# Optimization experiments

Hardware: AMD Instinct MI355X
Metric: run time of the kernel (lower is better)

## Reference

```python
import jax, jax.numpy as jnp
import numpy as np

G = 3040      # number of drugs / graph nodes in the drug-drug graph
A = 100       # atoms per molecular graph (smileNode, uniform)
TOK = 43      # token vocabulary (hard-coded in module)
FS = 75       # nfeat_smile
HS = 128      # nhid_smile
H1S = 128     # nhid1_smile
NF = 512      # nfeat (raw 384 + 128 smile emb)
NH = 256      # nhid
DH = 256      # dhid1


def setup_inputs() -> dict:
    key = jax.random.key(0)
    ks = jax.random.split(key, 20)
    s = 0.05
    inp = {
        "x": jax.random.normal(ks[0], (G, NF - H1S), dtype=jnp.float32),
        "adj_pos": jax.random.uniform(ks[1], (G, G), dtype=jnp.float32) / G,
        "adj_neg": jax.random.uniform(ks[2], (G, G), dtype=jnp.float32) / G,
        "mol_adj": jax.random.uniform(ks[3], (G, A, A), dtype=jnp.float32) / A,
        "encoded_drug": jax.random.randint(ks[4], (G, A), 0, TOK, dtype=jnp.int64),
        # learned params
        "tok_emb": jax.random.normal(ks[5], (TOK, FS), dtype=jnp.float32),
        "Wm1": jax.random.normal(ks[6], (G, FS, HS), dtype=jnp.float32) * s,
        "Wm2": jax.random.normal(ks[7], (G, HS, H1S), dtype=jnp.float32) * s,
        "Wp1": jax.random.normal(ks[8], (NF, NH), dtype=jnp.float32) * s,
        "Wp2": jax.random.normal(ks[9], (NH, NH), dtype=jnp.float32) * s,
        "Wn1": jax.random.normal(ks[10], (NF, NH), dtype=jnp.float32) * s,
        "Wn2": jax.random.normal(ks[11], (NH, NH), dtype=jnp.float32) * s,
        "Wd1": jax.random.normal(ks[12], (2 * NH, DH), dtype=jnp.float32) * s,
        "Wd2": jax.random.normal(ks[13], (DH, 2 * DH), dtype=jnp.float32) * s,
        "Wd3": jax.random.normal(ks[14], (2 * DH, DH), dtype=jnp.float32) * s,
        "Wdec": jax.random.normal(ks[15], (DH, DH), dtype=jnp.float32) * s,
    }
    return inp


def reference(x, adj_pos, adj_neg, mol_adj, encoded_drug, tok_emb,
              Wm1, Wm2, Wp1, Wp2, Wn1, Wn2, Wd1, Wd2, Wd3, Wdec):
    # --- calDrugSmileFeatures: batched over all 3040 per-graph GCN encoders ---
    feats = tok_emb[encoded_drug]                          # [G, A, FS] (embedding gather)
    h = jnp.einsum('gab,gaf,gfh->gbh', mol_adj, feats, Wm1)  # gc1: adj @ (x @ W1), per graph
    h = jnp.einsum('gab,gah,ghk->gbk', mol_adj, h, Wm2)      # gc2 (dropout inactive, eval)
    emb_drugs = jnp.max(h, axis=1)                          # [G, H1S] node-wise maxpool

    # --- main drug-drug graph ---
    xc = jnp.concatenate([x, emb_drugs], axis=1)            # [G, NF]
    hp = jax.nn.relu(adj_pos @ (xc @ Wp1))                  # GCNEncoder pos layer1
    zp = adj_pos @ (hp @ Wp2)                               # layer2
    hn = jax.nn.relu(adj_neg @ (xc @ Wn1))
    zn = adj_neg @ (hn @ Wn2)
    z = jnp.concatenate([zp, zn], axis=1)                   # [G, 2*NH]

    # --- DSN MLP (eval: dropout inactive) ---
    z = jax.nn.relu(z @ Wd1)
    z = jax.nn.relu(z @ Wd2)
    z = z @ Wd3                                             # [G, DH]

    # --- Bilinear decoder: z W z^T logits ---
    y_pred = (z @ Wdec) @ z.T                               # [G, G]
    return y_pred
```

## Files before the change

kernel.cpp:

```cpp
#include <hip/hip_runtime.h>
#include <cstdint>
#include <cstddef>

#define Gn   3040
#define An   100
#define TOKn 43
#define FSn  75
#define NFn  512
#define XC   384

typedef __attribute__((ext_vector_type(8))) short s16x8;
typedef __attribute__((ext_vector_type(4))) float f32x4;

__device__ __forceinline__ void split_bf16(float x, unsigned short &h, unsigned short &l)
{
  unsigned u = __float_as_uint(x);
  unsigned r = (u + 0x7fffu + ((u >> 16) & 1u)) & 0xffff0000u;
  h = (unsigned short)(r >> 16);
  float res = x - __uint_as_float(r);
  unsigned v = __float_as_uint(res);
  l = (unsigned short)((v + 0x7fffu + ((v >> 16) & 1u)) >> 16);
}

#define MFMA3(acc, ah, al, bh, bl)                                              \
  acc = __builtin_amdgcn_mfma_f32_16x16x32_bf16(ah, bh, acc, 0, 0, 0);          \
  acc = __builtin_amdgcn_mfma_f32_16x16x32_bf16(ah, bl, acc, 0, 0, 0);          \
  acc = __builtin_amdgcn_mfma_f32_16x16x32_bf16(al, bh, acc, 0, 0, 0);

__device__ __forceinline__ s16x8 tail_frag(const unsigned short* p, bool act)
{
  s16x8 f = {0,0,0,0,0,0,0,0};
  if (act) {
    uint2 v = *(const uint2*)p;
    f[0] = (short)(v.x & 0xffffu); f[1] = (short)(v.x >> 16);
    f[2] = (short)(v.y & 0xffffu); f[3] = (short)(v.y >> 16);
  }
  return f;
}

__device__ __forceinline__ void pack_split4(const f32x4 a, uint2 &ph, uint2 &pl)
{
  unsigned short h[4], l[4];
  #pragma unroll
  for (int r = 0; r < 4; ++r) split_bf16(a[r], h[r], l[r]);
  ph.x = (unsigned)h[0] | ((unsigned)h[1] << 16);
  ph.y = (unsigned)h[2] | ((unsigned)h[3] << 16);
  pl.x = (unsigned)l[0] | ((unsigned)l[1] << 16);
  pl.y = (unsigned)l[2] | ((unsigned)l[3] << 16);
}

__global__ void prep_tok_kernel(const float* __restrict__ tok_emb,
                                unsigned short* __restrict__ th,
                                unsigned short* __restrict__ tl)
{
  int i = blockIdx.x * 256 + threadIdx.x;
  if (i >= TOKn * 96) return;
  int r = i / 96, f = i % 96;
  float v = (f < FSn) ? tok_emb[r * FSn + f] : 0.f;
  unsigned short h, l;
  split_bf16(v, h, l);
  th[i] = h; tl[i] = l;
}

__global__ __launch_bounds__(256) void prep_w_kernel(
    const float* __restrict__ Wp1, const float* __restrict__ Wn1,
    const float* __restrict__ Wp2, const float* __restrict__ Wn2,
    const float* __restrict__ Wd1, const float* __restrict__ Wd2,
    const float* __restrict__ Wd3, const float* __restrict__ Wdec,
    unsigned short* __restrict__ WS)
{
  __shared__ float sT[32][33];
  const float* S; int K, N; unsigned off;
  switch (blockIdx.z) {
    case 0:  S = Wp1;  K = 512; N = 256; off = 0;       break;
    case 1:  S = Wn1;  K = 512; N = 256; off = 262144;  break;
    case 2:  S = Wp2;  K = 256; N = 256; off = 524288;  break;
    case 3:  S = Wn2;  K = 256; N = 256; off = 655360;  break;
    case 4:  S = Wd1;  K = 512; N = 256; off = 786432;  break;
    case 5:  S = Wd2;  K = 256; N = 512; off = 1048576; break;
    case 6:  S = Wd3;  K = 512; N = 256; off = 1310720; break;
    default: S = Wdec; K = 256; N = 256; off = 1572864; break;
  }
  const int r0 = blockIdx.x * 32, c0 = blockIdx.y * 32;
  if (r0 >= K || c0 >= N) return;
  unsigned short* H = WS + off;
  unsigned short* L = H + K * N;
  const int t = threadIdx.x;
  {
    const int i = t >> 3, j0 = (t & 7) * 4;
    float4 v = *(const float4*)&S[(size_t)(r0 + i) * N + c0 + j0];
    sT[i][j0] = v.x; sT[i][j0+1] = v.y; sT[i][j0+2] = v.z; sT[i][j0+3] = v.w;
  }
  __syncthreads();
  {
    const int jj = t >> 3, ii0 = (t & 7) * 4;
    unsigned short h[4], lo[4];
    #pragma unroll
    for (int q = 0; q < 4; ++q) split_bf16(sT[ii0 + q][jj], h[q], lo[q]);
    ushort4 hv = make_ushort4(h[0], h[1], h[2], h[3]);
    ushort4 lv = make_ushort4(lo[0], lo[1], lo[2], lo[3]);
    *(ushort4*)&H[(size_t)(c0 + jj) * K + r0 + ii0] = hv;
    *(ushort4*)&L[(size_t)(c0 + jj) * K + r0 + ii0] = lv;
  }
}

__global__ __launch_bounds__(1024, 1) void smile_mfma_kernel(
    const float* __restrict__ mol_adj, const int* __restrict__ enc,
    const unsigned short* __restrict__ tokh, const unsigned short* __restrict__ tokl,
    const float* __restrict__ Wm1, const float* __restrict__ Wm2,
    float* __restrict__ xc)
{
  __shared__ __align__(16) unsigned short sm[74624];
  __shared__ float sMax[8][2][16];
  unsigned short* adjT_h = sm;
  unsigned short* adjT_l = sm + 10400;
  unsigned short* bufA_h = sm + 20800;
  unsigned short* bufA_l = sm + 34112;
  unsigned short* g1_h   = sm + 47424;
  unsigned short* g1_l   = sm + 61024;
  float* Sf = (float*)(sm + 20800);

  const int g = blockIdx.x;
  const int t = threadIdx.x;
  const int w = t >> 6, l = t & 63;
  const int wc = w & 7, wr = w >> 3;
  const int lr = l & 15, lq = l >> 4;
  const int hcol = 16 * wc + lr;
  const int NI = wr ? 3 : 4;
  const int IB = wr * 4;
  const f32x4 z4 = {0.f, 0.f, 0.f, 0.f};
  const s16x8 z8 = {0,0,0,0,0,0,0,0};

  const float* adjg = mol_adj + (size_t)g * (An * An);
  #pragma unroll
  for (int j = 0; j < 3; ++j) {
    const int i = t + 1024 * j;
    if (i < 2500) {
      float4 v = *(const float4*)&adjg[i * 4];
      const int a = i / 25, c4 = (i % 25) * 4;
      float* p = &Sf[a * 101 + c4];
      p[0] = v.x; p[1] = v.y; p[2] = v.z; p[3] = v.w;
    }
  }
  __syncthreads();
  #pragma unroll
  for (int j = 0; j < 3; ++j) {
    const int i = t + 1024 * j;
    if (i < 2500) {
      const int b = i / 25, a4 = (i % 25) * 4;
      f32x4 v;
      #pragma unroll
      for (int q = 0; q < 4; ++q) v[q] = Sf[(a4 + q) * 101 + b];
      uint2 ph, pl;
      pack_split4(v, ph, pl);
      *(uint2*)&adjT_h[b * 104 + a4] = ph;
      *(uint2*)&adjT_l[b * 104 + a4] = pl;
    }
  }
  __syncthreads();

  {
    const float* W1 = Wm1 + (size_t)g * (FSn * 128);
    s16x8 bh[3], bl[3];
    #pragma unroll
    for (int kc = 0; kc < 3; ++kc)
      #pragma unroll
      for (int j = 0; j < 8; ++j) {
        const int f = 32 * kc + 8 * lq + j;
        float v = (f < FSn) ? W1[f * 128 + hcol] : 0.f;
        unsigned short hh, ll;
        split_bf16(v, hh, ll);
        bh[kc][j] = (short)hh; bl[kc][j] = (short)ll;
      }
    f32x4 acc[4];
    #pragma unroll
    for (int i = 0; i < 4; ++i) acc[i] = z4;
    #pragma unroll
    for (int m2 = 0; m2 < 4; ++m2) {
      if (m2 < NI) {
        const int mi = IB + m2;
        const int a = 16 * mi + lr;
        const bool va = a < An;
        const int tk = va ? enc[g * An + a] : 0;
        const unsigned short* th = tokh + tk * 96 + 8 * lq;
        const unsigned short* tl = tokl + tk * 96 + 8 * lq;
        #pragma unroll
        for (int kc = 0; kc < 3; ++kc) {
          s16x8 ah = z8, al = z8;
          if (va) { ah = *(const s16x8*)&th[32 * kc]; al = *(const s16x8*)&tl[32 * kc]; }
          MFMA3(acc[m2], ah, al, bh[kc], bl[kc]);
        }
      }
    }
    #pragma unroll
    for (int m2 = 0; m2 < 4; ++m2) {
      if (m2 < NI) {
        const int a0 = 16 * (IB + m2) + 4 * lq;
        if (a0 < An) {
          uint2 ph, pl;
          pack_split4(acc[m2], ph, pl);
          *(uint2*)&bufA_h[hcol * 104 + a0] = ph;
          *(uint2*)&bufA_l[hcol * 104 + a0] = pl;
        }
      }
    }
  }
  __syncthreads();

  {
    const unsigned short* xh = &bufA_h[hcol * 104];
    const unsigned short* xl = &bufA_l[hcol * 104];
    f32x4 acc[4];
    #pragma unroll
    for (int i = 0; i < 4; ++i) acc[i] = z4;
    #pragma unroll
    for (int kc = 0; kc < 4; ++kc) {
      s16x8 ah, al;
      if (kc < 3) {
        ah = *(const s16x8*)&xh[32 * kc + 8 * lq];
        al = *(const s16x8*)&xl[32 * kc + 8 * lq];
      } else {
        ah = tail_frag(xh + 96, lq == 0);
        al = tail_frag(xl + 96, lq == 0);
      }
      #pragma unroll
      for (int n2 = 0; n2 < 4; ++n2) {
        if (n2 < NI) {
          const int b = 16 * (IB + n2) + lr;
          const bool vb = b < An;
          s16x8 bh = z8, bl = z8;
          if (kc < 3) {
            if (vb) {
              bh = *(const s16x8*)&adjT_h[b * 104 + 32 * kc + 8 * lq];
              bl = *(const s16x8*)&adjT_l[b * 104 + 32 * kc + 8 * lq];
            }
          } else {
            bh = tail_frag(&adjT_h[b * 104 + 96], vb && lq == 0);
            bl = tail_frag(&adjT_l[b * 104 + 96], vb && lq == 0);
          }
          MFMA3(acc[n2], ah, al, bh, bl);
        }
      }
    }
    #pragma unroll
    for (int n2 = 0; n2 < 4; ++n2) {
      if (n2 < NI) {
        const int b = 16 * (IB + n2) + lr;
        if (b < An) {
          uint2 ph, pl;
          pack_split4(acc[n2], ph, pl);
          *(uint2*)&g1_h[b * 136 + 16 * wc + 4 * lq] = ph;
          *(uint2*)&g1_l[b * 136 + 16 * wc + 4 * lq] = pl;
        }
      }
    }
  }
  __syncthreads();

  {
    const float* W2 = Wm2 + (size_t)g * (128 * 128);
    s16x8 bh[4], bl[4];
    #pragma unroll
    for (int kc = 0; kc < 4; ++kc)
      #pragma unroll
      for (int j = 0; j < 8; ++j) {
        unsigned short hh, ll;
        split_bf16(W2[(32 * kc + 8 * lq + j) * 128 + hcol], hh, ll);
        bh[kc][j] = (short)hh; bl[kc][j] = (short)ll;
      }
    f32x4 acc[4];
    #pragma unroll
    for (int i = 0; i < 4; ++i) acc[i] = z4;
    #pragma unroll
    for (int kc = 0; kc < 4; ++kc) {
      #pragma unroll
      for (int m2 = 0; m2 < 4; ++m2) {
        if (m2 < NI) {
          const int b = 16 * (IB + m2) + lr;
          const bool vb = b < An;
          s16x8 ah = z8, al = z8;
          if (vb) {
            ah = *(const s16x8*)&g1_h[b * 136 + 32 * kc + 8 * lq];
            al = *(const s16x8*)&g1_l[b * 136 + 32 * kc + 8 * lq];
          }
          MFMA3(acc[m2], ah, al, bh[kc], bl[kc]);
        }
      }
    }
    #pragma unroll
    for (int m2 = 0; m2 < 4; ++m2) {
      if (m2 < NI) {
        const int b0 = 16 * (IB + m2) + 4 * lq;
        if (b0 < An) {
          uint2 ph, pl;
          pack_split4(acc[m2], ph, pl);
          *(uint2*)&bufA_h[hcol * 104 + b0] = ph;
          *(uint2*)&bufA_l[hcol * 104 + b0] = pl;
        }
      }
    }
  }
  __syncthreads();

  {
    const unsigned short* fh = &bufA_h[hcol * 104];
    const unsigned short* fl = &bufA_l[hcol * 104];
    f32x4 acc[4];
    #pragma unroll
    for (int i = 0; i < 4; ++i) acc[i] = z4;
    #pragma unroll
    for (int kc = 0; kc < 4; ++kc) {
      s16x8 ah, al;
      if (kc < 3) {
        ah = *(const s16x8*)&fh[32 * kc + 8 * lq];
        al = *(const s16x8*)&fl[32 * kc + 8 * lq];
      } else {
        ah = tail_frag(fh + 96, lq == 0);
        al = tail_frag(fl + 96, lq == 0);
      }
      #pragma unroll
      for (int n2 = 0; n2 < 4; ++n2) {
        if (n2 < NI) {
          const int b = 16 * (IB + n2) + lr;
          const bool vb = b < An;
          s16x8 bh = z8, bl = z8;
          if (kc < 3) {
            if (vb) {
              bh = *(const s16x8*)&adjT_h[b * 104 + 32 * kc + 8 * lq];
              bl = *(const s16x8*)&adjT_l[b * 104 + 32 * kc + 8 * lq];
            }
          } else {
            bh = tail_frag(&adjT_h[b * 104 + 96], vb && lq == 0);
            bl = tail_frag(&adjT_l[b * 104 + 96], vb && lq == 0);
          }
          MFMA3(acc[n2], ah, al, bh, bl);
        }
      }
    }
    float mr[4] = {-3.4e38f, -3.4e38f, -3.4e38f, -3.4e38f};
    #pragma unroll
    for (int n2 = 0; n2 < 4; ++n2) {
      if (n2 < NI && (16 * (IB + n2) + lr) < An) {
        #pragma unroll
        for (int r = 0; r < 4; ++r) mr[r] = fmaxf(mr[r], acc[n2][r]);
      }
    }
    #pragma unroll
    for (int d = 1; d < 16; d <<= 1) {
      #pragma unroll
      for (int r = 0; r < 4; ++r) mr[r] = fmaxf(mr[r], __shfl_xor(mr[r], d, 64));
    }
    if (lr == 0) {
      #pragma unroll
      for (int r = 0; r < 4; ++r) sMax[wc][wr][4 * lq + r] = mr[r];
    }
  }
  __syncthreads();
  if (wr == 0 && lr == 0) {
    #pragma unroll
    for (int r = 0; r < 4; ++r) {
      const int h = 16 * wc + 4 * lq + r;
      xc[(size_t)g * NFn + XC + h] =
          fmaxf(sMax[wc][0][4 * lq + r], sMax[wc][1][4 * lq + r]);
    }
  }
}

template<bool SPLIT, bool BF32>
__global__ __launch_bounds__(256, 2) void mgemm_kernel(
    const float* __restrict__ A0, const float* __restrict__ A1,
    const unsigned short* __restrict__ Bh0, const unsigned short* __restrict__ Bl0,
    const unsigned short* __restrict__ Bh1, const unsigned short* __restrict__ Bl1,
    const float* __restrict__ Bf,
    float* __restrict__ C0, float* __restrict__ C1,
    int M, int N, int K)
{
  __shared__ __align__(16) unsigned short lds[16384];

  const int z = blockIdx.z;
  int pair, k0base, kend;
  if (SPLIT) {
    pair = z & 1;
    int s = z >> 1;
    k0base = s * 768;
    kend = k0base + 768; if (kend > K) kend = K;
  } else { pair = 0; k0base = 0; kend = K; }

  const float* A = pair ? A1 : A0;
  const unsigned short* Bh = pair ? Bh1 : Bh0;
  const unsigned short* Bl = pair ? Bl1 : Bl0;
  float* C;
  if (SPLIT) C = (pair ? C1 : C0) + (size_t)(z >> 1) * M * N;
  else       C = C0;

  const int t  = threadIdx.x;
  const int l  = t & 63;
  const int wv = t >> 6;
  const int wr = wv >> 1, wc = wv & 1;
  const int m0 = blockIdx.x * 128, n0 = blockIdx.y * 128;

  const int sm = (t >> 6) * 16 + (t & 15);
  const int sk = ((t >> 4) & 3) * 8;

  const f32x4 zero4 = {0.f, 0.f, 0.f, 0.f};
  f32x4 acc[4][4];
  #pragma unroll
  for (int i = 0; i < 4; ++i)
    #pragma unroll
    for (int j = 0; j < 4; ++j) acc[i][j] = zero4;

  for (int k0 = k0base; k0 < kend; k0 += 32) {
    float4 a00 = make_float4(0.f,0.f,0.f,0.f), a01 = a00, a10 = a00, a11 = a00;
    {
      const size_t base = (size_t)(m0 + sm) * K + k0 + sk;
      if (m0 + sm < M)      { a00 = *(const float4*)&A[base];
                              a01 = *(const float4*)&A[base + 4]; }
      if (m0 + sm + 64 < M) { a10 = *(const float4*)&A[base + (size_t)64 * K];
                              a11 = *(const float4*)&A[base + (size_t)64 * K + 4]; }
    }
    s16x8 b0h, b0l, b1h, b1l;
    float4 bf00, bf01, bf10, bf11;
    if (BF32) {
      bf00 = make_float4(0.f,0.f,0.f,0.f); bf01 = bf00; bf10 = bf00; bf11 = bf00;
      const size_t base = (size_t)(n0 + sm) * K + k0 + sk;
      if (n0 + sm < N)      { bf00 = *(const float4*)&Bf[base];
                              bf01 = *(const float4*)&Bf[base + 4]; }
      if (n0 + sm + 64 < N) { bf10 = *(const float4*)&Bf[base + (size_t)64 * K];
                              bf11 = *(const float4*)&Bf[base + (size_t)64 * K + 4]; }
    } else {
      const size_t base = (size_t)(n0 + sm) * K + k0 + sk;
      b0h = *(const s16x8*)&Bh[base];
      b0l = *(const s16x8*)&Bl[base];
      b1h = *(const s16x8*)&Bh[base + (size_t)64 * K];
      b1l = *(const s16x8*)&Bl[base + (size_t)64 * K];
    }

    s16x8 a0h, a0l, a1h, a1l;
    {
      const float av0[8] = {a00.x,a00.y,a00.z,a00.w,a01.x,a01.y,a01.z,a01.w};
      const float av1[8] = {a10.x,a10.y,a10.z,a10.w,a11.x,a11.y,a11.z,a11.w};
      #pragma unroll
      for (int j = 0; j < 8; ++j) {
        unsigned short hh, ll;
        split_bf16(av0[j], hh, ll); a0h[j] = (short)hh; a0l[j] = (short)ll;
        split_bf16(av1[j], hh, ll); a1h[j] = (short)hh; a1l[j] = (short)ll;
      }
    }
    if (BF32) {
      const float bv0[8] = {bf00.x,bf00.y,bf00.z,bf00.w,bf01.x,bf01.y,bf01.z,bf01.w};
      const float bv1[8] = {bf10.x,bf10.y,bf10.z,bf10.w,bf11.x,bf11.y,bf11.z,bf11.w};
      #pragma unroll
      for (int j = 0; j < 8; ++j) {
        unsigned short hh, ll;
        split_bf16(bv0[j], hh, ll); b0h[j] = (short)hh; b0l[j] = (short)ll;
        split_bf16(bv1[j], hh, ll); b1h[j] = (short)hh; b1l[j] = (short)ll;
      }
    }

    __syncthreads();
    {
      const int sl = (t & 63) * 8;
      const int c1 = t >> 6, c2 = c1 + 4;
      *(s16x8*)&lds[c1 * 512 + sl]          = a0h;
      *(s16x8*)&lds[4096 + c1 * 512 + sl]   = a0l;
      *(s16x8*)&lds[c2 * 512 + sl]          = a1h;
      *(s16x8*)&lds[4096 + c2 * 512 + sl]   = a1l;
      *(s16x8*)&lds[8192  + c1 * 512 + sl]  = b0h;
      *(s16x8*)&lds[12288 + c1 * 512 + sl]  = b0l;
      *(s16x8*)&lds[8192  + c2 * 512 + sl]  = b1h;
      *(s16x8*)&lds[12288 + c2 * 512 + sl]  = b1l;
    }
    __syncthreads();

    s16x8 vbh[4], vbl[4];
    #pragma unroll
    for (int ni = 0; ni < 4; ++ni) {
      const int c = wc * 4 + ni;
      vbh[ni] = *(const s16x8*)&lds[8192  + c * 512 + l * 8];
      vbl[ni] = *(const s16x8*)&lds[12288 + c * 512 + l * 8];
    }
    #pragma unroll
    for (int mi = 0; mi < 4; ++mi) {
      const int c = wr * 4 + mi;
      s16x8 ah = *(const s16x8*)&lds[c * 512 + l * 8];
      s16x8 al = *(const s16x8*)&lds[4096 + c * 512 + l * 8];
      #pragma unroll
      for (int ni = 0; ni < 4; ++ni) {
        acc[mi][ni] = __builtin_amdgcn_mfma_f32_16x16x32_bf16(ah, vbh[ni], acc[mi][ni], 0, 0, 0);
        acc[mi][ni] = __builtin_amdgcn_mfma_f32_16x16x32_bf16(ah, vbl[ni], acc[mi][ni], 0, 0, 0);
        acc[mi][ni] = __builtin_amdgcn_mfma_f32_16x16x32_bf16(al, vbh[ni], acc[mi][ni], 0, 0, 0);
      }
    }
  }

  #pragma unroll
  for (int mi = 0; mi < 4; ++mi) {
    const int rowb = m0 + (wr * 4 + mi) * 16 + (l >> 4) * 4;
    #pragma unroll
    for (int ni = 0; ni < 4; ++ni) {
      const int col = n0 + (wc * 4 + ni) * 16 + (l & 15);
      if (col < N) {
        #pragma unroll
        for (int r = 0; r < 4; ++r) {
          const int row = rowb + r;
          if (row < M) C[(size_t)row * N + col] = acc[mi][ni][r];
        }
      }
    }
  }
}

template<int EOUT>
__global__ __launch_bounds__(256, 2) void wgemm_kernel(
    const float* __restrict__ A0, const float* __restrict__ A1,
    const unsigned short* __restrict__ Bh0, const unsigned short* __restrict__ Bl0,
    const unsigned short* __restrict__ Bh1, const unsigned short* __restrict__ Bl1,
    float* __restrict__ C0, float* __restrict__ C1,
    unsigned short* __restrict__ H0, unsigned short* __restrict__ L0,
    unsigned short* __restrict__ H1, unsigned short* __restrict__ L1,
    int M, int N, int K)
{
  __shared__ __align__(16) unsigned short lds[16384];

  const int pair = blockIdx.z;
  const float* A = pair ? A1 : A0;
  const unsigned short* Bh = pair ? Bh1 : Bh0;
  const unsigned short* Bl = pair ? Bl1 : Bl0;

  const int t  = threadIdx.x;
  const int l  = t & 63;
  const int wv = t >> 6;
  const int wr = wv >> 1, wc = wv & 1;
  const int m0 = blockIdx.x * 128, n0 = blockIdx.y * 128;

  const int sm = (t >> 6) * 16 + (t & 15);
  const int sk = ((t >> 4) & 3) * 8;

  const f32x4 zero4 = {0.f, 0.f, 0.f, 0.f};
  f32x4 acc[4][4];
  #pragma unroll
  for (int i = 0; i < 4; ++i)
    #pragma unroll
    for (int j = 0; j < 4; ++j) acc[i][j] = zero4;

  for (int k0 = 0; k0 < K; k0 += 32) {
    float4 a00 = make_float4(0.f,0.f,0.f,0.f), a01 = a00, a10 = a00, a11 = a00;
    {
      const size_t base = (size_t)(m0 + sm) * K + k0 + sk;
      if (m0 + sm < M)      { a00 = *(const float4*)&A[base];
                              a01 = *(const float4*)&A[base + 4]; }
      if (m0 + sm + 64 < M) { a10 = *(const float4*)&A[base + (size_t)64 * K];
                              a11 = *(const float4*)&A[base + (size_t)64 * K + 4]; }
    }
    s16x8 b0h, b0l, b1h, b1l;
    {
      const size_t base = (size_t)(n0 + sm) * K + k0 + sk;
      b0h = *(const s16x8*)&Bh[base];
      b0l = *(const s16x8*)&Bl[base];
      b1h = *(const s16x8*)&Bh[base + (size_t)64 * K];
      b1l = *(const s16x8*)&Bl[base + (size_t)64 * K];
    }
    s16x8 a0h, a0l, a1h, a1l;
    {
      const float av0[8] = {a00.x,a00.y,a00.z,a00.w,a01.x,a01.y,a01.z,a01.w};
      const float av1[8] = {a10.x,a10.y,a10.z,a10.w,a11.x,a11.y,a11.z,a11.w};
      #pragma unroll
      for (int j = 0; j < 8; ++j) {
        unsigned short hh, ll;
        split_bf16(av0[j], hh, ll); a0h[j] = (short)hh; a0l[j] = (short)ll;
        split_bf16(av1[j], hh, ll); a1h[j] = (short)hh; a1l[j] = (short)ll;
      }
    }

    __syncthreads();
    {
      const int sl = (t & 63) * 8;
      const int c1 = t >> 6, c2 = c1 + 4;
      *(s16x8*)&lds[c1 * 512 + sl]          = a0h;
      *(s16x8*)&lds[4096 + c1 * 512 + sl]   = a0l;
      *(s16x8*)&lds[c2 * 512 + sl]          = a1h;
      *(s16x8*)&lds[4096 + c2 * 512 + sl]   = a1l;
      *(s16x8*)&lds[8192  + c1 * 512 + sl]  = b0h;
      *(s16x8*)&lds[12288 + c1 * 512 + sl]  = b0l;
      *(s16x8*)&lds[8192  + c2 * 512 + sl]  = b1h;
      *(s16x8*)&lds[12288 + c2 * 512 + sl]  = b1l;
    }
    __syncthreads();

    s16x8 vbh[4], vbl[4];
    #pragma unroll
    for (int ni = 0; ni < 4; ++ni) {
      const int c = wc * 4 + ni;
      vbh[ni] = *(const s16x8*)&lds[8192  + c * 512 + l * 8];
      vbl[ni] = *(const s16x8*)&lds[12288 + c * 512 + l * 8];
    }
    #pragma unroll
    for (int mi = 0; mi < 4; ++mi) {
      const int c = wr * 4 + mi;
      s16x8 ah = *(const s16x8*)&lds[c * 512 + l * 8];
      s16x8 al = *(const s16x8*)&lds[4096 + c * 512 + l * 8];
      #pragma unroll
      for (int ni = 0; ni < 4; ++ni) {
        acc[mi][ni] = __builtin_amdgcn_mfma_f32_16x16x32_bf16(ah, vbh[ni], acc[mi][ni], 0, 0, 0);
        acc[mi][ni] = __builtin_amdgcn_mfma_f32_16x16x32_bf16(ah, vbl[ni], acc[mi][ni], 0, 0, 0);
        acc[mi][ni] = __builtin_amdgcn_mfma_f32_16x16x32_bf16(al, vbh[ni], acc[mi][ni], 0, 0, 0);
      }
    }
  }

  if (EOUT <= 1) {
    float* C = pair ? C1 : C0;
    #pragma unroll
    for (int mi = 0; mi < 4; ++mi) {
      const int rowb = m0 + (wr * 4 + mi) * 16 + (l >> 4) * 4;
      #pragma unroll
      for (int ni = 0; ni < 4; ++ni) {
        const int col = n0 + (wc * 4 + ni) * 16 + (l & 15);
        if (col < N) {
          #pragma unroll
          for (int r = 0; r < 4; ++r) {
            const int row = rowb + r;
            if (row < M) {
              float v = acc[mi][ni][r];
              if (EOUT == 1) v = fmaxf(v, 0.f);
              C[(size_t)row * N + col] = v;
            }
          }
        }
      }
    }
  } else {
    unsigned short* H = pair ? H1 : H0;
    unsigned short* L = pair ? L1 : L0;
    #pragma unroll
    for (int mi = 0; mi < 4; ++mi) {
      const int rowb = m0 + (wr * 4 + mi) * 16 + (l >> 4) * 4;
      if (rowb < M) {
        #pragma unroll
        for (int ni = 0; ni < 4; ++ni) {
          const int col = n0 + (wc * 4 + ni) * 16 + (l & 15);
          if (col < N) {
            uint2 ph, pl;
            pack_split4(acc[mi][ni], ph, pl);
            *(uint2*)&H[(size_t)col * M + rowb] = ph;
            *(uint2*)&L[(size_t)col * M + rowb] = pl;
          }
        }
      }
    }
  }
}

__global__ void reduce_kernel(const float* __restrict__ part, float* __restrict__ dst,
                              int S, int M, int N, int ldc, int coff, int relu)
{
  int i = blockIdx.x * blockDim.x + threadIdx.x;
  int total = M * (N / 4);
  if (i >= total) return;
  int r = i / (N / 4), c = (i % (N / 4)) * 4;
  float4 s = make_float4(0.f, 0.f, 0.f, 0.f);
  for (int j = 0; j < S; ++j) {
    float4 v = *(const float4*)&part[(size_t)j * M * N + (size_t)r * N + c];
    s.x += v.x; s.y += v.y; s.z += v.z; s.w += v.w;
  }
  if (relu) {
    s.x = fmaxf(s.x, 0.f); s.y = fmaxf(s.y, 0.f);
    s.z = fmaxf(s.z, 0.f); s.w = fmaxf(s.w, 0.f);
  }
  *(float4*)&dst[(size_t)r * ldc + coff + c] = s;
}

__global__ void copyx_kernel(const float* __restrict__ x, float* __restrict__ xc)
{
  int i = blockIdx.x * blockDim.x + threadIdx.x;
  int total = Gn * (XC / 4);
  if (i >= total) return;
  int r = i / (XC / 4), c = (i % (XC / 4)) * 4;
  *(float4*)&xc[(size_t)r * NFn + c] = *(const float4*)&x[(size_t)r * XC + c];
}

extern "C" void kernel_launch(void* const* d_in, const int* in_sizes, int n_in,
                              void* d_out, int out_size, void* d_ws, size_t ws_size,
                              hipStream_t stream)
{
  const float* x       = (const float*)d_in[0];
  const float* adj_pos = (const float*)d_in[1];
  const float* adj_neg = (const float*)d_in[2];
  const float* mol_adj = (const float*)d_in[3];
  const int*   enc     = (const int*)d_in[4];
  const float* tok_emb = (const float*)d_in[5];
  const float* Wm1     = (const float*)d_in[6];
  const float* Wm2     = (const float*)d_in[7];
  const float* Wp1     = (const float*)d_in[8];
  const float* Wp2     = (const float*)d_in[9];
  const float* Wn1     = (const float*)d_in[10];
  const float* Wn2     = (const float*)d_in[11];
  const float* Wd1     = (const float*)d_in[12];
  const float* Wd2     = (const float*)d_in[13];
  const float* Wd3     = (const float*)d_in[14];
  const float* Wdec    = (const float*)d_in[15];
  float* out = (float*)d_out;
  float* ws  = (float*)d_ws;

  const size_t MN  = (size_t)Gn * 256;
  const size_t MN2 = (size_t)Gn * 512;
  size_t o = 0;
  float* xc    = ws + o; o += MN2;
  float* P1    = ws + o; o += MN;
  float* N1    = ws + o; o += MN;
  float* hp    = ws + o; o += MN;
  float* hn    = ws + o; o += MN;
  float* P2    = ws + o; o += MN;
  float* N2    = ws + o; o += MN;
  float* zbuf  = ws + o; o += MN2;
  float* d1    = ws + o; o += MN;
  float* d2    = ws + o; o += MN2;
  float* z3    = ws + o; o += MN;
  float* tb    = ws + o; o += MN;
  float* partP = ws + o; o += 4 * MN;
  float* partN = ws + o; o += 4 * MN;
  unsigned short* tokh = (unsigned short*)(ws + o);
  unsigned short* tokl = tokh + TOKn * 96; o += 4128;
  unsigned short* WS = (unsigned short*)(ws + o); o += 851968;
  unsigned short* Wp1s  = WS + 0;
  unsigned short* Wn1s  = WS + 262144;
  unsigned short* Wp2s  = WS + 524288;
  unsigned short* Wn2s  = WS + 655360;
  unsigned short* Wd1s  = WS + 786432;
  unsigned short* Wd2s  = WS + 1048576;
  unsigned short* Wd3s  = WS + 1310720;
  unsigned short* Wdecs = WS + 1572864;

  unsigned short* BTPh = (unsigned short*)d2;
  unsigned short* BTPl = BTPh + (size_t)256 * Gn;
  unsigned short* BTNh = BTPh + (size_t)2 * 256 * Gn;
  unsigned short* BTNl = BTPh + (size_t)3 * 256 * Gn;

  dim3 b256(256);

  prep_tok_kernel<<<dim3((TOKn * 96 + 255) / 256), b256, 0, stream>>>(tok_emb, tokh, tokl);
  prep_w_kernel<<<dim3(16, 16, 8), b256, 0, stream>>>(
      Wp1, Wn1, Wp2, Wn2, Wd1, Wd2, Wd3, Wdec, WS);
  copyx_kernel<<<dim3((Gn * (XC / 4) + 255) / 256), b256, 0, stream>>>(x, xc);
  smile_mfma_kernel<<<dim3(Gn), dim3(1024), 0, stream>>>(
      mol_adj, enc, tokh, tokl, Wm1, Wm2, xc);
  wgemm_kernel<2><<<dim3(24, 2, 2), b256, 0, stream>>>(
      xc, xc, Wp1s, Wp1s + 131072, Wn1s, Wn1s + 131072,
      nullptr, nullptr, BTPh, BTPl, BTNh, BTNl, Gn, 256, 512);
  mgemm_kernel<true, false><<<dim3(24, 2, 8), b256, 0, stream>>>(
      adj_pos, adj_neg, BTPh, BTPl, BTNh, BTNl, (const float*)nullptr,
      partP, partN, Gn, 256, Gn);
  reduce_kernel<<<dim3(760), b256, 0, stream>>>(partP, hp, 4, Gn, 256, 256, 0, 1);
  reduce_kernel<<<dim3(760), b256, 0, stream>>>(partN, hn, 4, Gn, 256, 256, 0, 1);
  wgemm_kernel<2><<<dim3(24, 2, 2), b256, 0, stream>>>(
      hp, hn, Wp2s, Wp2s + 65536, Wn2s, Wn2s + 65536,
      nullptr, nullptr, BTPh, BTPl, BTNh, BTNl, Gn, 256, 256);
  mgemm_kernel<true, false><<<dim3(24, 2, 8), b256, 0, stream>>>(
      adj_pos, adj_neg, BTPh, BTPl, BTNh, BTNl, (const float*)nullptr,
      partP, partN, Gn, 256, Gn);
  reduce_kernel<<<dim3(760), b256, 0, stream>>>(partP, zbuf, 4, Gn, 256, 512, 0, 0);
  reduce_kernel<<<dim3(760), b256, 0, stream>>>(partN, zbuf, 4, Gn, 256, 512, 256, 0);
  wgemm_kernel<1><<<dim3(24, 2, 1), b256, 0, stream>>>(
      zbuf, zbuf, Wd1s, Wd1s + 131072, Wd1s, Wd1s + 131072,
      d1, d1, nullptr, nullptr, nullptr, nullptr, Gn, 256, 512);
  wgemm_kernel<1><<<dim3(24, 4, 1), b256, 0, stream>>>(
      d1, d1, Wd2s, Wd2s + 131072, Wd2s, Wd2s + 131072,
      d2, d2, nullptr, nullptr, nullptr, nullptr, Gn, 512, 256);
  wgemm_kernel<0><<<dim3(24, 2, 1), b256, 0, stream>>>(
      d2, d2, Wd3s, Wd3s + 131072, Wd3s, Wd3s + 131072,
      z3, z3, nullptr, nullptr, nullptr, nullptr, Gn, 256, 512);
  wgemm_kernel<0><<<dim3(24, 2, 1), b256, 0, stream>>>(
      z3, z3, Wdecs, Wdecs + 65536, Wdecs, Wdecs + 65536,
      tb, tb, nullptr, nullptr, nullptr, nullptr, Gn, 256, 256);
  mgemm_kernel<false, true><<<dim3(24, 24, 1), b256, 0, stream>>>(
      tb, tb, (const unsigned short*)nullptr, (const unsigned short*)nullptr,
      (const unsigned short*)nullptr, (const unsigned short*)nullptr,
      z3, out, out, Gn, Gn, 256);
}
```

Measured before the change: 966.1 us.

## Use hardware packed bf16 conversion for splits and presplit bilinear decoder operands

Replaces the software round-to-nearest fp32→bf16 hi/lo split with the packed v_cvt_pk_bf16_f32 instruction in every kernel, cutting the ALU work of operand conversion. The final z·Wdec·zᵀ GEMM now runs on a new pgemm kernel. A separate presplit pass converts tb and z3 to bf16 hi/lo arrays once, so the GEMM no longer re-splits fp32 tiles in each of its 576 blocks. This adds an extra launch plus scratch traffic in the partP buffer. The new GEMM also reads up to 3072 rows without bounds checks, past the 3040 valid rows.

```diff
diff --git a/kernel.cpp b/kernel.cpp
--- a/kernel.cpp
+++ b/kernel.cpp
@@ -11,15 +11,42 @@
 
 typedef __attribute__((ext_vector_type(8))) short s16x8;
 typedef __attribute__((ext_vector_type(4))) float f32x4;
-
-__device__ __forceinline__ void split_bf16(float x, unsigned short &h, unsigned short &l)
-{
-  unsigned u = __float_as_uint(x);
-  unsigned r = (u + 0x7fffu + ((u >> 16) & 1u)) & 0xffff0000u;
-  h = (unsigned short)(r >> 16);
-  float res = x - __uint_as_float(r);
-  unsigned v = __float_as_uint(res);
-  l = (unsigned short)((v + 0x7fffu + ((v >> 16) & 1u)) >> 16);
+typedef __attribute__((ext_vector_type(4))) unsigned u32x4;
+
+__device__ __forceinline__ unsigned cvt2(float a, float b)
+{
+  unsigned r;
+  asm("v_cvt_pk_bf16_f32 %0, %1, %2" : "=v"(r) : "v"(a), "v"(b));
+  return r;
+}
+
+__device__ __forceinline__ void split2(float a, float b, unsigned &hw, unsigned &lw)
+{
+  hw = cvt2(a, b);
+  float ra = a - __uint_as_float(hw << 16);
+  float rb = b - __uint_as_float(hw & 0xffff0000u);
+  lw = cvt2(ra, rb);
+}
+
+__device__ __forceinline__ void split8(const float* v, s16x8 &h, s16x8 &l)
+{
+  union { s16x8 s; u32x4 u; } H, L;
+  #pragma unroll
+  for (int q = 0; q < 4; ++q) {
+    unsigned hw, lw;
+    split2(v[2*q], v[2*q+1], hw, lw);
+    H.u[q] = hw; L.u[q] = lw;
+  }
+  h = H.s; l = L.s;
+}
+
+__device__ __forceinline__ void pack_split4(const f32x4 a, uint2 &ph, uint2 &pl)
+{
+  unsigned h0, l0, h1, l1;
+  split2(a[0], a[1], h0, l0);
+  split2(a[2], a[3], h1, l1);
+  ph.x = h0; ph.y = h1;
+  pl.x = l0; pl.y = l1;
 }
 
 #define MFMA3(acc, ah, al, bh, bl)                                              \
@@ -38,17 +65,6 @@
   return f;
 }
 
-__device__ __forceinline__ void pack_split4(const f32x4 a, uint2 &ph, uint2 &pl)
-{
-  unsigned short h[4], l[4];
-  #pragma unroll
-  for (int r = 0; r < 4; ++r) split_bf16(a[r], h[r], l[r]);
-  ph.x = (unsigned)h[0] | ((unsigned)h[1] << 16);
-  ph.y = (unsigned)h[2] | ((unsigned)h[3] << 16);
-  pl.x = (unsigned)l[0] | ((unsigned)l[1] << 16);
-  pl.y = (unsigned)l[2] | ((unsigned)l[3] << 16);
-}
-
 __global__ void prep_tok_kernel(const float* __restrict__ tok_emb,
                                 unsigned short* __restrict__ th,
                                 unsigned short* __restrict__ tl)
@@ -57,9 +73,10 @@
   if (i >= TOKn * 96) return;
   int r = i / 96, f = i % 96;
   float v = (f < FSn) ? tok_emb[r * FSn + f] : 0.f;
-  unsigned short h, l;
-  split_bf16(v, h, l);
-  th[i] = h; tl[i] = l;
+  unsigned hw, lw;
+  split2(v, 0.f, hw, lw);
+  th[i] = (unsigned short)(hw & 0xffffu);
+  tl[i] = (unsigned short)(lw & 0xffffu);
 }
 
 __global__ __launch_bounds__(256) void prep_w_kernel(
@@ -94,14 +111,33 @@
   __syncthreads();
   {
     const int jj = t >> 3, ii0 = (t & 7) * 4;
-    unsigned short h[4], lo[4];
-    #pragma unroll
-    for (int q = 0; q < 4; ++q) split_bf16(sT[ii0 + q][jj], h[q], lo[q]);
-    ushort4 hv = make_ushort4(h[0], h[1], h[2], h[3]);
-    ushort4 lv = make_ushort4(lo[0], lo[1], lo[2], lo[3]);
-    *(ushort4*)&H[(size_t)(c0 + jj) * K + r0 + ii0] = hv;
-    *(ushort4*)&L[(size_t)(c0 + jj) * K + r0 + ii0] = lv;
-  }
+    f32x4 v;
+    #pragma unroll
+    for (int q = 0; q < 4; ++q) v[q] = sT[ii0 + q][jj];
+    uint2 ph, pl;
+    pack_split4(v, ph, pl);
+    *(uint2*)&H[(size_t)(c0 + jj) * K + r0 + ii0] = ph;
+    *(uint2*)&L[(size_t)(c0 + jj) * K + r0 + ii0] = pl;
+  }
+}
+
+__global__ __launch_bounds__(256) void presplit_kernel(
+    const float* __restrict__ S0, const float* __restrict__ S1,
+    unsigned short* __restrict__ H0, unsigned short* __restrict__ L0,
+    unsigned short* __restrict__ H1, unsigned short* __restrict__ L1, int n8)
+{
+  int i = blockIdx.x * 256 + threadIdx.x;
+  if (i >= n8) return;
+  const float* S     = blockIdx.y ? S1 : S0;
+  unsigned short* H  = blockIdx.y ? H1 : H0;
+  unsigned short* L  = blockIdx.y ? L1 : L0;
+  float4 v0 = *(const float4*)&S[i * 8];
+  float4 v1 = *(const float4*)&S[i * 8 + 4];
+  const float v[8] = {v0.x, v0.y, v0.z, v0.w, v1.x, v1.y, v1.z, v1.w};
+  s16x8 h, l;
+  split8(v, h, l);
+  *(s16x8*)&H[i * 8] = h;
+  *(s16x8*)&L[i * 8] = l;
 }
 
 __global__ __launch_bounds__(1024, 1) void smile_mfma_kernel(
@@ -163,15 +199,15 @@
     const float* W1 = Wm1 + (size_t)g * (FSn * 128);
     s16x8 bh[3], bl[3];
     #pragma unroll
-    for (int kc = 0; kc < 3; ++kc)
+    for (int kc = 0; kc < 3; ++kc) {
+      float wv[8];
       #pragma unroll
       for (int j = 0; j < 8; ++j) {
         const int f = 32 * kc + 8 * lq + j;
-        float v = (f < FSn) ? W1[f * 128 + hcol] : 0.f;
-        unsigned short hh, ll;
-        split_bf16(v, hh, ll);
-        bh[kc][j] = (short)hh; bl[kc][j] = (short)ll;
-      }
+        wv[j] = (f < FSn) ? W1[f * 128 + hcol] : 0.f;
+      }
+      split8(wv, bh[kc], bl[kc]);
+    }
     f32x4 acc[4];
     #pragma unroll
     for (int i = 0; i < 4; ++i) acc[i] = z4;
@@ -261,13 +297,13 @@
     const float* W2 = Wm2 + (size_t)g * (128 * 128);
     s16x8 bh[4], bl[4];
     #pragma unroll
-    for (int kc = 0; kc < 4; ++kc)
-      #pragma unroll
-      for (int j = 0; j < 8; ++j) {
-        unsigned short hh, ll;
-        split_bf16(W2[(32 * kc + 8 * lq + j) * 128 + hcol], hh, ll);
-        bh[kc][j] = (short)hh; bl[kc][j] = (short)ll;
-      }
+    for (int kc = 0; kc < 4; ++kc) {
+      float wv[8];
+      #pragma unroll
+      for (int j = 0; j < 8; ++j)
+        wv[j] = W2[(32 * kc + 8 * lq + j) * 128 + hcol];
+      split8(wv, bh[kc], bl[kc]);
+    }
     f32x4 acc[4];
     #pragma unroll
     for (int i = 0; i < 4; ++i) acc[i] = z4;
@@ -439,22 +475,14 @@
     {
       const float av0[8] = {a00.x,a00.y,a00.z,a00.w,a01.x,a01.y,a01.z,a01.w};
       const float av1[8] = {a10.x,a10.y,a10.z,a10.w,a11.x,a11.y,a11.z,a11.w};
-      #pragma unroll
-      for (int j = 0; j < 8; ++j) {
-        unsigned short hh, ll;
-        split_bf16(av0[j], hh, ll); a0h[j] = (short)hh; a0l[j] = (short)ll;
-        split_bf16(av1[j], hh, ll); a1h[j] = (short)hh; a1l[j] = (short)ll;
-      }
+      split8(av0, a0h, a0l);
+      split8(av1, a1h, a1l);
     }
     if (BF32) {
       const float bv0[8] = {bf00.x,bf00.y,bf00.z,bf00.w,bf01.x,bf01.y,bf01.z,bf01.w};
       const float bv1[8] = {bf10.x,bf10.y,bf10.z,bf10.w,bf11.x,bf11.y,bf11.z,bf11.w};
-      #pragma unroll
-      for (int j = 0; j < 8; ++j) {
-        unsigned short hh, ll;
-        split_bf16(bv0[j], hh, ll); b0h[j] = (short)hh; b0l[j] = (short)ll;
-        split_bf16(bv1[j], hh, ll); b1h[j] = (short)hh; b1l[j] = (short)ll;
-      }
+      split8(bv0, b0h, b0l);
+      split8(bv1, b1h, b1l);
     }
 
     __syncthreads();
@@ -510,6 +538,99 @@
   }
 }
 
+__global__ __launch_bounds__(256, 2) void pgemm_kernel(
+    const unsigned short* __restrict__ Ah, const unsigned short* __restrict__ Al,
+    const unsigned short* __restrict__ Bh, const unsigned short* __restrict__ Bl,
+    float* __restrict__ C, int M, int N, int K)
+{
+  __shared__ __align__(16) unsigned short lds[16384];
+
+  const int t  = threadIdx.x;
+  const int l  = t & 63;
+  const int wv = t >> 6;
+  const int wr = wv >> 1, wc = wv & 1;
+  const int m0 = blockIdx.x * 128, n0 = blockIdx.y * 128;
+
+  const int sm = (t >> 6) * 16 + (t & 15);
+  const int sk = ((t >> 4) & 3) * 8;
+
+  const f32x4 zero4 = {0.f, 0.f, 0.f, 0.f};
+  f32x4 acc[4][4];
+  #pragma unroll
+  for (int i = 0; i < 4; ++i)
+    #pragma unroll
+    for (int j = 0; j < 4; ++j) acc[i][j] = zero4;
+
+  for (int k0 = 0; k0 < K; k0 += 32) {
+    s16x8 a0h, a0l, a1h, a1l, b0h, b0l, b1h, b1l;
+    {
+      const size_t base = (size_t)(m0 + sm) * K + k0 + sk;
+      a0h = *(const s16x8*)&Ah[base];
+      a0l = *(const s16x8*)&Al[base];
+      a1h = *(const s16x8*)&Ah[base + (size_t)64 * K];
+      a1l = *(const s16x8*)&Al[base + (size_t)64 * K];
+    }
+    {
+      const size_t base = (size_t)(n0 + sm) * K + k0 + sk;
+      b0h = *(const s16x8*)&Bh[base];
+      b0l = *(const s16x8*)&Bl[base];
+      b1h = *(const s16x8*)&Bh[base + (size_t)64 * K];
+      b1l = *(const s16x8*)&Bl[base + (size_t)64 * K];
+    }
+
+    __syncthreads();
+    {
+      const int sl = (t & 63) * 8;
+      const int c1 = t >> 6, c2 = c1 + 4;
+      *(s16x8*)&lds[c1 * 512 + sl]          = a0h;
+      *(s16x8*)&lds[4096 + c1 * 512 + sl]   = a0l;
+      *(s16x8*)&lds[c2 * 512 + sl]          = a1h;
+      *(s16x8*)&lds[4096 + c2 * 512 + sl]   = a1l;
+      *(s16x8*)&lds[8192  + c1 * 512 + sl]  = b0h;
+      *(s16x8*)&lds[12288 + c1 * 512 + sl]  = b0l;
+      *(s16x8*)&lds[8192  + c2 * 512 + sl]  = b1h;
+      *(s16x8*)&lds[12288 + c2 * 512 + sl]  = b1l;
+    }
+    __syncthreads();
+
+    s16x8 vbh[4], vbl[4];
+    #pragma unroll
+    for (int ni = 0; ni < 4; ++ni) {
+      const int c = wc * 4 + ni;
+      vbh[ni] = *(const s16x8*)&lds[8192  + c * 512 + l * 8];
+      vbl[ni] = *(const s16x8*)&lds[12288 + c * 512 + l * 8];
+    }
+    #pragma unroll
+    for (int mi = 0; mi < 4; ++mi) {
+      const int c = wr * 4 + mi;
+      s16x8 ah = *(const s16x8*)&lds[c * 512 + l * 8];
+      s16x8 al = *(const s16x8*)&lds[4096 + c * 512 + l * 8];
+      #pragma unroll
+      for (int ni = 0; ni < 4; ++ni) {
+        acc[mi][ni] = __builtin_amdgcn_mfma_f32_16x16x32_bf16(ah, vbh[ni], acc[mi][ni], 0, 0, 0);
+        acc[mi][ni] = __builtin_amdgcn_mfma_f32_16x16x32_bf16(ah, vbl[ni], acc[mi][ni], 0, 0, 0);
+        acc[mi][ni] = __builtin_amdgcn_mfma_f32_16x16x32_bf16(al, vbh[ni], acc[mi][ni], 0, 0, 0);
+      }
+    }
+  }
+
+  #pragma unroll
+  for (int mi = 0; mi < 4; ++mi) {
+    const int rowb = m0 + (wr * 4 + mi) * 16 + (l >> 4) * 4;
+    #pragma unroll
+    for (int ni = 0; ni < 4; ++ni) {
+      const int col = n0 + (wc * 4 + ni) * 16 + (l & 15);
+      if (col < N) {
+        #pragma unroll
+        for (int r = 0; r < 4; ++r) {
+          const int row = rowb + r;
+          if (row < M) C[(size_t)row * N + col] = acc[mi][ni][r];
+        }
+      }
+    }
+  }
+}
+
 template<int EOUT>
 __global__ __launch_bounds__(256, 2) void wgemm_kernel(
     const float* __restrict__ A0, const float* __restrict__ A1,
@@ -564,12 +685,8 @@
     {
       const float av0[8] = {a00.x,a00.y,a00.z,a00.w,a01.x,a01.y,a01.z,a01.w};
       const float av1[8] = {a10.x,a10.y,a10.z,a10.w,a11.x,a11.y,a11.z,a11.w};
-      #pragma unroll
-      for (int j = 0; j < 8; ++j) {
-        unsigned short hh, ll;
-        split_bf16(av0[j], hh, ll); a0h[j] = (short)hh; a0l[j] = (short)ll;
-        split_bf16(av1[j], hh, ll); a1h[j] = (short)hh; a1l[j] = (short)ll;
-      }
+      split8(av0, a0h, a0l);
+      split8(av1, a1h, a1l);
     }
 
     __syncthreads();
@@ -735,6 +852,11 @@
   unsigned short* BTPl = BTPh + (size_t)256 * Gn;
   unsigned short* BTNh = BTPh + (size_t)2 * 256 * Gn;
   unsigned short* BTNl = BTPh + (size_t)3 * 256 * Gn;
+
+  unsigned short* tbh = (unsigned short*)partP;
+  unsigned short* tbl = tbh + (size_t)Gn * 256;
+  unsigned short* z3h = tbh + (size_t)2 * Gn * 256;
+  unsigned short* z3l = tbh + (size_t)3 * Gn * 256;
 
   dim3 b256(256);
 
@@ -772,8 +894,8 @@
   wgemm_kernel<0><<<dim3(24, 2, 1), b256, 0, stream>>>(
       z3, z3, Wdecs, Wdecs + 65536, Wdecs, Wdecs + 65536,
       tb, tb, nullptr, nullptr, nullptr, nullptr, Gn, 256, 256);
-  mgemm_kernel<false, true><<<dim3(24, 24, 1), b256, 0, stream>>>(
-      tb, tb, (const unsigned short*)nullptr, (const unsigned short*)nullptr,
-      (const unsigned short*)nullptr, (const unsigned short*)nullptr,
-      z3, out, out, Gn, Gn, 256);
-}
+  presplit_kernel<<<dim3((Gn * 256 / 8 + 255) / 256, 2), b256, 0, stream>>>(
+      tb, z3, tbh, tbl, z3h, z3l, Gn * 256 / 8);
+  pgemm_kernel<<<dim3(24, 24, 1), b256, 0, stream>>>(
+      tbh, tbl, z3h, z3l, out, Gn, Gn, 256);
+}
```

Result: faster. 922.8 us (-4.5%).
